# Optimization experiments

Hardware: AMD Instinct MI355X
Metric: run time of the kernel (lower is better)

Reference implementation:

```python
import jax, jax.numpy as jnp
import numpy as np

ALPHA = 0.2      # GAT leaky_relu slope (args.alpha)
MLP_SLOPE = 0.01 # F.leaky_relu default in the MLP path
NEG = -9e15

def _l2_normalize(x, axis=1, eps=1e-12):
    n = jnp.sqrt(jnp.sum(x * x, axis=axis, keepdims=True))
    return x / jnp.maximum(n, eps)

def setup_inputs() -> dict:
    key = jax.random.key(0)
    ks = jax.random.split(key, 14)
    N, Din, Dh, H, Dg, M1, M2, E = 8192, 512, 256, 2, 512, 512, 256, 100000
    x = jax.random.normal(ks[0], (N, Din), dtype=jnp.float32)
    adj = jax.random.randint(ks[1], (N, N), 0, 2, dtype=jnp.int32)
    train_sample = jax.random.randint(ks[2], (E, 2), 0, N, dtype=jnp.int32)
    llm_emb = jax.random.normal(ks[3], (N, Dg), dtype=jnp.float32)
    # GAT head params (stacked over heads)
    Wg = jax.random.normal(ks[4], (H, Din, Dh), dtype=jnp.float32) * 0.05
    a1 = jax.random.normal(ks[5], (H, Dh), dtype=jnp.float32) * 0.05
    a2 = jax.random.normal(ks[6], (H, Dh), dtype=jnp.float32) * 0.05
    bias_g = jnp.zeros((H, Dh), dtype=jnp.float32)
    # MLP params
    W1 = jax.random.normal(ks[7], (Dh + Dg, M1), dtype=jnp.float32) * 0.03
    b1 = jnp.zeros((M1,), dtype=jnp.float32)
    W2 = jax.random.normal(ks[8], (M1, M2), dtype=jnp.float32) * 0.04
    b2 = jnp.zeros((M2,), dtype=jnp.float32)
    return {"x": x, "adj": adj, "train_sample": train_sample, "llm_emb": llm_emb,
            "Wg": Wg, "a1": a1, "a2": a2, "bias_g": bias_g,
            "W1": W1, "b1": b1, "W2": W2, "b2": b2}

def reference(x, adj, train_sample, llm_emb, Wg, a1, a2, bias_g, W1, b1, W2, b2):
    mask = adj > 0  # [N, N]

    def head(W, av1, av2, b):
        h = x @ W                                   # [N, Dh]
        s1 = h @ av1                                # [N]
        s2 = h @ av2                                # [N]
        e = jax.nn.leaky_relu(s1[:, None] + s2[None, :], ALPHA)  # [N, N]
        att = jax.nn.softmax(jnp.where(mask, e, NEG), axis=1)
        out = att @ h                               # [N, Dh]
        out = jax.nn.leaky_relu(out, ALPHA)
        out = _l2_normalize(out, axis=1)
        return out + b

    # encode: single GNN layer -> mean over heads (dropout inactive in eval)
    out_heads = jax.vmap(head)(Wg, a1, a2, bias_g)  # [H, N, Dh]
    embed_gnn = jnp.mean(out_heads, axis=0)         # [N, Dh]
    embed = jnp.concatenate([llm_emb, embed_gnn], axis=1)  # [N, Dg+Dh]

    def mlp(z):
        z = jax.nn.leaky_relu(z @ W1 + b1, MLP_SLOPE)
        z = jax.nn.leaky_relu(z @ W2 + b2, MLP_SLOPE)
        return z

    tf_embed = mlp(embed)
    target_embed = mlp(embed)
    train_tf = tf_embed[train_sample[:, 0]]
    train_tg = target_embed[train_sample[:, 1]]
    pred = jnp.sum(train_tf * train_tg, axis=1, keepdims=True)  # dot decode, [E,1]
    return pred
```

## Files before the change

### kernel.cpp

```cpp
#include <hip/hip_runtime.h>
#include <hip/hip_bf16.h>
#include <cstdint>
#include <cstddef>

#define ALPHA 0.2f
#define MLP_SLOPE 0.01f

typedef short bf16x8 __attribute__((ext_vector_type(8)));
typedef float f32x4 __attribute__((ext_vector_type(4)));
typedef unsigned short ushort_t;

#define ASM_BARRIER() __asm__ __volatile__("s_waitcnt lgkmcnt(0)\n\ts_barrier" ::: "memory")

__device__ __forceinline__ float lrelu(float x, float s) { return x > 0.f ? x : x * s; }
__device__ __forceinline__ ushort_t f2bf(float x) {
  __hip_bfloat16 h = __float2bfloat16(x);
  return *reinterpret_cast<ushort_t*>(&h);
}
__device__ __forceinline__ float bf2f(ushort_t u) {
  union { unsigned int i; float f; } v; v.i = ((unsigned int)u) << 16; return v.f;
}

__global__ __launch_bounds__(256) void tobf(
    const float* __restrict__ in, ushort_t* __restrict__ outp)
{
  int idx = blockIdx.x * 256 + threadIdx.x;
  float4 v = ((const float4*)in)[idx];
  ushort4 h;
  h.x = f2bf(v.x); h.y = f2bf(v.y); h.z = f2bf(v.z); h.w = f2bf(v.w);
  ((ushort4*)outp)[idx] = h;
}

__global__ __launch_bounds__(256) void zero_f(float* __restrict__ p)
{
  int idx = blockIdx.x * 256 + threadIdx.x;
  ((float4*)p)[idx] = make_float4(0.f, 0.f, 0.f, 0.f);
}

__global__ __launch_bounds__(256) void pack_wt(
    const float* __restrict__ W, ushort_t* __restrict__ hi,
    ushort_t* __restrict__ lo, int K, int N)
{
  int gid = blockIdx.x * 256 + threadIdx.x;
  int lane = gid & 63;
  int kbc = K >> 5;
  int kblk = (gid >> 6) % kbc;
  int nblk = (gid >> 6) / kbc;
  size_t b = (size_t)blockIdx.y * K * N;
  int col = nblk * 16 + (lane & 15);
  int krow = kblk * 32 + (lane >> 4) * 8;
  ushort_t h[8] __attribute__((aligned(16)));
  ushort_t l[8] __attribute__((aligned(16)));
#pragma unroll
  for (int e = 0; e < 8; ++e) {
    float v = W[b + (size_t)(krow + e) * N + col];
    h[e] = f2bf(v);
    l[e] = f2bf(v - bf2f(h[e]));
  }
  *(uint4*)&hi[b + (size_t)gid * 8] = *(uint4*)h;
  if (lo) *(uint4*)&lo[b + (size_t)gid * 8] = *(uint4*)l;
}

__global__ __launch_bounds__(256, 2) void gemm_h(
    const ushort_t* __restrict__ xb, const ushort_t* __restrict__ Wgp,
    const float* __restrict__ a1, const float* __restrict__ a2,
    ushort_t* __restrict__ Bpack, float* __restrict__ s1,
    float* __restrict__ s2)
{
  __shared__ ushort_t Ab[2][128][40];
  const int t = threadIdx.x;
  const int head = blockIdx.z;
  const int m0 = blockIdx.y * 128;
  const int n0 = blockIdx.x * 64;
  const int wave = t >> 6;
  const int wm = (wave & 1) * 64, wn = (wave >> 1) * 32;
  const int l16 = t & 15, quad = (t >> 4) & 3, l63 = t & 63;
  const int sr = t >> 1, sp = (t & 1) * 16;
  const ushort_t* arow_g = xb + (size_t)(m0 + sr) * 512 + sp;
  const ushort_t* bp = Wgp + (size_t)head * 256 * 512;
  const int nb0 = (n0 + wn) >> 4;

  f32x4 acc[4][2];
#pragma unroll
  for (int i = 0; i < 4; ++i)
#pragma unroll
    for (int j = 0; j < 2; ++j) acc[i][j] = (f32x4){0.f, 0.f, 0.f, 0.f};

  uint4 r0, r1;
  r0 = *(const uint4*)(arow_g);
  r1 = *(const uint4*)(arow_g + 8);
  *(uint4*)&Ab[0][sr][sp] = r0;
  *(uint4*)&Ab[0][sr][sp + 8] = r1;
  __syncthreads();

  for (int kb = 0; kb < 16; ++kb) {
    const int cur = kb & 1, nxt = cur ^ 1;
    if (kb < 15) {
      const ushort_t* p = arow_g + (kb + 1) * 32;
      r0 = *(const uint4*)p;
      r1 = *(const uint4*)(p + 8);
    }
    bf16x8 Bf[2];
#pragma unroll
    for (int nt = 0; nt < 2; ++nt)
      Bf[nt] = *(const bf16x8*)&bp[(((size_t)(nb0 + nt) * 16 + kb) * 64 + l63) * 8];
    bf16x8 Af[4];
#pragma unroll
    for (int mt = 0; mt < 4; ++mt)
      Af[mt] = *(const bf16x8*)&Ab[cur][wm + mt * 16 + l16][quad * 8];
#pragma unroll
    for (int mt = 0; mt < 4; ++mt)
#pragma unroll
      for (int nt = 0; nt < 2; ++nt)
        acc[mt][nt] = __builtin_amdgcn_mfma_f32_16x16x32_bf16(
            Af[mt], Bf[nt], acc[mt][nt], 0, 0, 0);
    if (kb < 15) {
      *(uint4*)&Ab[nxt][sr][sp] = r0;
      *(uint4*)&Ab[nxt][sr][sp + 8] = r1;
    }
    __syncthreads();
  }

#pragma unroll
  for (int mt = 0; mt < 4; ++mt)
#pragma unroll
    for (int nt = 0; nt < 2; ++nt)
#pragma unroll
      for (int rg = 0; rg < 4; ++rg) {
        int j = m0 + wm + mt * 16 + quad * 4 + rg;
        int c = n0 + wn + nt * 16 + l16;
        int kblk = j >> 5;
        int laneb = ((j >> 3) & 3) * 16 + (c & 15);
        int e = j & 7;
        Bpack[(((size_t)head * 256 + kblk) * 16 + (c >> 4)) * 512 + laneb * 8 + e] =
            f2bf(acc[mt][nt][rg]);
      }
  float a1v[2], a2v[2];
#pragma unroll
  for (int nt = 0; nt < 2; ++nt) {
    int c = n0 + wn + nt * 16 + l16;
    a1v[nt] = a1[head * 256 + c];
    a2v[nt] = a2[head * 256 + c];
  }
#pragma unroll
  for (int mt = 0; mt < 4; ++mt)
#pragma unroll
    for (int rg = 0; rg < 4; ++rg) {
      float p1 = acc[mt][0][rg] * a1v[0] + acc[mt][1][rg] * a1v[1];
      float p2 = acc[mt][0][rg] * a2v[0] + acc[mt][1][rg] * a2v[1];
      p1 += __shfl_xor(p1, 1); p2 += __shfl_xor(p2, 1);
      p1 += __shfl_xor(p1, 2); p2 += __shfl_xor(p2, 2);
      p1 += __shfl_xor(p1, 4); p2 += __shfl_xor(p2, 4);
      p1 += __shfl_xor(p1, 8); p2 += __shfl_xor(p2, 8);
      if (l16 == 0) {
        int row = m0 + wm + mt * 16 + quad * 4 + rg;
        atomicAdd(&s1[head * 8192 + row], p1);
        atomicAdd(&s2[head * 8192 + row], p2);
      }
    }
}

__global__ __launch_bounds__(256, 2) void gemm_mlp(
    const ushort_t* __restrict__ Ahi, const ushort_t* __restrict__ Alo,
    const ushort_t* __restrict__ Bph, const ushort_t* __restrict__ Bpl,
    const float* __restrict__ bias, float* __restrict__ Cf,
    ushort_t* __restrict__ Chi, ushort_t* __restrict__ Clo,
    int M, int N, int K, float slope)
{
  __shared__ ushort_t Ah[2][128][40], Al[2][128][40];
  const int kbc = K >> 5;
  const int t = threadIdx.x;
  const int m0 = blockIdx.y * 128;
  const int n0 = blockIdx.x * 64;
  const int wave = t >> 6;
  const int wm = (wave & 1) * 64, wn = (wave >> 1) * 32;
  const int l16 = t & 15, quad = (t >> 4) & 3, l63 = t & 63;
  const int sr = t >> 1, sp = (t & 1) * 16;
  const ushort_t* ah_g = Ahi + (size_t)(m0 + sr) * K + sp;
  const ushort_t* al_g = Alo + (size_t)(m0 + sr) * K + sp;
  const int nb0 = (n0 + wn) >> 4;

  f32x4 acc[4][2];
#pragma unroll
  for (int i = 0; i < 4; ++i)
#pragma unroll
    for (int j = 0; j < 2; ++j) acc[i][j] = (f32x4){0.f, 0.f, 0.f, 0.f};

  uint4 rh0, rh1, rl0, rl1;
  rh0 = *(const uint4*)(ah_g);
  rh1 = *(const uint4*)(ah_g + 8);
  rl0 = *(const uint4*)(al_g);
  rl1 = *(const uint4*)(al_g + 8);
  *(uint4*)&Ah[0][sr][sp] = rh0;
  *(uint4*)&Ah[0][sr][sp + 8] = rh1;
  *(uint4*)&Al[0][sr][sp] = rl0;
  *(uint4*)&Al[0][sr][sp + 8] = rl1;
  __syncthreads();

  for (int kb = 0; kb < kbc; ++kb) {
    const int cur = kb & 1, nxt = cur ^ 1;
    if (kb + 1 < kbc) {
      const ushort_t* ph = ah_g + (kb + 1) * 32;
      const ushort_t* plo = al_g + (kb + 1) * 32;
      rh0 = *(const uint4*)ph;
      rh1 = *(const uint4*)(ph + 8);
      rl0 = *(const uint4*)plo;
      rl1 = *(const uint4*)(plo + 8);
    }
    bf16x8 bh[2], bl[2];
#pragma unroll
    for (int nt = 0; nt < 2; ++nt) {
      size_t o = (((size_t)(nb0 + nt) * kbc + kb) * 64 + l63) * 8;
      bh[nt] = *(const bf16x8*)&Bph[o];
      bl[nt] = *(const bf16x8*)&Bpl[o];
    }
    bf16x8 afh[4], afl[4];
#pragma unroll
    for (int mt = 0; mt < 4; ++mt) {
      afh[mt] = *(const bf16x8*)&Ah[cur][wm + mt * 16 + l16][quad * 8];
      afl[mt] = *(const bf16x8*)&Al[cur][wm + mt * 16 + l16][quad * 8];
    }
#pragma unroll
    for (int mt = 0; mt < 4; ++mt)
#pragma unroll
      for (int nt = 0; nt < 2; ++nt) {
        acc[mt][nt] = __builtin_amdgcn_mfma_f32_16x16x32_bf16(afh[mt], bh[nt], acc[mt][nt], 0, 0, 0);
        acc[mt][nt] = __builtin_amdgcn_mfma_f32_16x16x32_bf16(afh[mt], bl[nt], acc[mt][nt], 0, 0, 0);
        acc[mt][nt] = __builtin_amdgcn_mfma_f32_16x16x32_bf16(afl[mt], bh[nt], acc[mt][nt], 0, 0, 0);
      }
    if (kb + 1 < kbc) {
      *(uint4*)&Ah[nxt][sr][sp] = rh0;
      *(uint4*)&Ah[nxt][sr][sp + 8] = rh1;
      *(uint4*)&Al[nxt][sr][sp] = rl0;
      *(uint4*)&Al[nxt][sr][sp + 8] = rl1;
    }
    __syncthreads();
  }

#pragma unroll
  for (int mt = 0; mt < 4; ++mt)
#pragma unroll
    for (int nt = 0; nt < 2; ++nt)
#pragma unroll
      for (int rg = 0; rg < 4; ++rg) {
        int m = m0 + wm + mt * 16 + quad * 4 + rg;
        int n = n0 + wn + nt * 16 + l16;
        float v = lrelu(acc[mt][nt][rg] + bias[n], slope);
        size_t o = (size_t)m * N + n;
        if (Cf) Cf[o] = v;
        if (Chi) {
          ushort_t h = f2bf(v);
          Chi[o] = h; Clo[o] = f2bf(v - bf2f(h));
        }
      }
}

__global__ __launch_bounds__(512, 1) void attn_mfma8(
    const ushort_t* __restrict__ Bpack, const float* __restrict__ s1g,
    const float* __restrict__ s2g, const int* __restrict__ adj,
    ushort_t* __restrict__ pacc, float* __restrict__ pl)
{
  __shared__ ushort_t Wlds[2][2][8][64][8];
  const int t = threadIdx.x;
  const int i0 = blockIdx.x * 128;
  const int js = blockIdx.y;
  const int kbase = js * 2048;
  const int wr = t >> 2, kq = t & 3;
  const int glane = kq * 16 + (wr & 15);
  const int gmt = wr >> 4;
  const float s1v0 = s1g[i0 + wr];
  const float s1v1 = s1g[8192 + i0 + wr];
  const int wave = t >> 6;
  const int head = wave >> 2, nh = (wave >> 1) & 1, rg2 = wave & 1;
  const int l16 = t & 15, quad = (t >> 4) & 3;
  const int l63 = t & 63;
  f32x4 acc[4][8];
#pragma unroll
  for (int m = 0; m < 4; ++m)
#pragma unroll
    for (int n = 0; n < 8; ++n) acc[m][n] = (f32x4){0.f, 0.f, 0.f, 0.f};
  float rs0 = 0.f, rs1 = 0.f;

  const int* arow = adj + (size_t)(i0 + wr) * 8192;
  int4 pa0, pa1;
  float4 p20a, p20b, p21a, p21b;

  auto fetch = [&](int kk) {
    pa0 = *(const int4*)&arow[kk];
    pa1 = *(const int4*)&arow[kk + 4];
    p20a = *(const float4*)&s2g[kk];
    p20b = *(const float4*)&s2g[kk + 4];
    p21a = *(const float4*)&s2g[8192 + kk];
    p21b = *(const float4*)&s2g[8192 + kk + 4];
  };
  auto gen = [&](int buf) {
    int am[8] = {pa0.x, pa0.y, pa0.z, pa0.w, pa1.x, pa1.y, pa1.z, pa1.w};
    float s20[8] = {p20a.x, p20a.y, p20a.z, p20a.w, p20b.x, p20b.y, p20b.z, p20b.w};
    float s21[8] = {p21a.x, p21a.y, p21a.z, p21a.w, p21b.x, p21b.y, p21b.z, p21b.w};
    ushort_t w0[8] __attribute__((aligned(16)));
    ushort_t w1[8] __attribute__((aligned(16)));
#pragma unroll
    for (int e = 0; e < 8; ++e) {
      float e0 = s1v0 + s20[e];
      float e1 = s1v1 + s21[e];
      e0 = fmaxf(e0, 0.f) + ALPHA * fminf(e0, 0.f);
      e1 = fmaxf(e1, 0.f) + ALPHA * fminf(e1, 0.f);
      float v0 = am[e] > 0 ? __expf(e0) : 0.f;
      float v1 = am[e] > 0 ? __expf(e1) : 0.f;
      rs0 += v0; rs1 += v1;
      w0[e] = f2bf(v0); w1[e] = f2bf(v1);
    }
    *(uint4*)&Wlds[buf][0][gmt][glane][0] = *(uint4*)w0;
    *(uint4*)&Wlds[buf][1][gmt][glane][0] = *(uint4*)w1;
  };

  fetch(kbase + kq * 8);
  gen(0);
  fetch(kbase + 32 + kq * 8);
  ASM_BARRIER();

  for (int kt = 0; kt < 64; ++kt) {
    const int cur = kt & 1, nxt = cur ^ 1;
    const int kblk = js * 64 + kt;
    const ushort_t* bb =
        Bpack + ((((size_t)head * 256 + kblk) * 16 + nh * 8) * 64 + l63) * 8;
    bf16x8 Bf[8];
#pragma unroll
    for (int nt = 0; nt < 8; ++nt)
      Bf[nt] = *(const bf16x8*)&bb[nt * 512];
    bf16x8 Af[4];
#pragma unroll
    for (int mt = 0; mt < 4; ++mt)
      Af[mt] = *(const bf16x8*)&Wlds[cur][head][rg2 * 4 + mt][l63][0];
#pragma unroll
    for (int mt = 0; mt < 4; ++mt)
#pragma unroll
      for (int nt = 0; nt < 8; ++nt)
        acc[mt][nt] = __builtin_amdgcn_mfma_f32_16x16x32_bf16(
            Af[mt], Bf[nt], acc[mt][nt], 0, 0, 0);
    if (kt < 63) {
      gen(nxt);
      if (kt < 62) fetch(kbase + (kt + 2) * 32 + kq * 8);
    }
    ASM_BARRIER();
  }

  rs0 += __shfl_xor(rs0, 1); rs0 += __shfl_xor(rs0, 2);
  rs1 += __shfl_xor(rs1, 1); rs1 += __shfl_xor(rs1, 2);
  if (kq == 0) {
    pl[((size_t)js * 2 + 0) * 8192 + i0 + wr] = rs0;
    pl[((size_t)js * 2 + 1) * 8192 + i0 + wr] = rs1;
  }
  const int n0 = nh * 128;
#pragma unroll
  for (int mt = 0; mt < 4; ++mt)
#pragma unroll
    for (int nt = 0; nt < 8; ++nt)
#pragma unroll
      for (int rg = 0; rg < 4; ++rg) {
        int row = i0 + rg2 * 64 + mt * 16 + quad * 4 + rg;
        int col = n0 + nt * 16 + l16;
        pacc[(((size_t)js * 2 + head) * 8192 + row) * 256 + col] =
            f2bf(acc[mt][nt][rg]);
      }
}

__global__ __launch_bounds__(256) void attn_finalize(
    const ushort_t* __restrict__ pacc, const float* __restrict__ pl,
    const float* __restrict__ bg, const float* __restrict__ llm,
    ushort_t* __restrict__ ehi, ushort_t* __restrict__ elo)
{
  __shared__ float red[8];
  const int r = blockIdx.x;
  const int t = threadIdx.x;
  const int wv = t >> 6, lane = t & 63;
#pragma unroll
  for (int half = 0; half < 2; ++half) {
    float lv = llm[(size_t)r * 512 + half * 256 + t];
    ushort_t h = f2bf(lv);
    ehi[(size_t)r * 768 + half * 256 + t] = h;
    elo[(size_t)r * 768 + half * 256 + t] = f2bf(lv - bf2f(h));
  }
  float o[2];
#pragma unroll
  for (int hh = 0; hh < 2; ++hh) {
    float num = 0.f, l = 0.f;
#pragma unroll
    for (int js = 0; js < 4; ++js) {
      num += bf2f(pacc[(((size_t)js * 2 + hh) * 8192 + r) * 256 + t]);
      l += pl[((size_t)js * 2 + hh) * 8192 + r];
    }
    o[hh] = lrelu(num / l, ALPHA);
  }
  float v0 = o[0] * o[0], v1 = o[1] * o[1];
  for (int off = 32; off > 0; off >>= 1) {
    v0 += __shfl_xor(v0, off);
    v1 += __shfl_xor(v1, off);
  }
  if (lane == 0) { red[wv] = v0; red[4 + wv] = v1; }
  __syncthreads();
  float n0 = fmaxf(sqrtf(red[0] + red[1] + red[2] + red[3]), 1e-12f);
  float n1 = fmaxf(sqrtf(red[4] + red[5] + red[6] + red[7]), 1e-12f);
  float val = 0.5f * (o[0] / n0 + bg[t] + o[1] / n1 + bg[256 + t]);
  ushort_t h = f2bf(val);
  ehi[(size_t)r * 768 + 512 + t] = h;
  elo[(size_t)r * 768 + 512 + t] = f2bf(val - bf2f(h));
}

__global__ __launch_bounds__(256) void pred_kernel(
    const float* __restrict__ z2, const int* __restrict__ ts,
    float* __restrict__ out, int E)
{
  const int gw = (blockIdx.x * 256 + threadIdx.x) >> 6;
  const int lane = threadIdx.x & 63;
  if (gw >= E) return;
  const int a = ts[gw * 2], b = ts[gw * 2 + 1];
  float4 va = ((const float4*)(z2 + (size_t)a * 256))[lane];
  float4 vb = ((const float4*)(z2 + (size_t)b * 256))[lane];
  float p = va.x * vb.x + va.y * vb.y + va.z * vb.z + va.w * vb.w;
  for (int off = 32; off > 0; off >>= 1) p += __shfl_xor(p, off);
  if (lane == 0) out[gw] = p;
}

extern "C" void kernel_launch(void* const* d_in, const int* in_sizes, int n_in,
                              void* d_out, int out_size, void* d_ws, size_t ws_size,
                              hipStream_t stream) {
  const float* x   = (const float*)d_in[0];
  const int*   adj = (const int*)d_in[1];
  const int*   ts  = (const int*)d_in[2];
  const float* llm = (const float*)d_in[3];
  const float* Wg  = (const float*)d_in[4];
  const float* a1  = (const float*)d_in[5];
  const float* a2  = (const float*)d_in[6];
  const float* bg  = (const float*)d_in[7];
  const float* W1  = (const float*)d_in[8];
  const float* b1  = (const float*)d_in[9];
  const float* W2  = (const float*)d_in[10];
  const float* b2  = (const float*)d_in[11];
  float* out = (float*)d_out;
  float* ws  = (float*)d_ws;
  const int E = in_sizes[2] / 2;

  ushort_t* xb    = (ushort_t*)(ws + 0);
  ushort_t* Wgp   = (ushort_t*)(ws + 2097152);
  ushort_t* W1ph  = (ushort_t*)(ws + 2228224);
  ushort_t* W1pl  = (ushort_t*)(ws + 2424832);
  ushort_t* W2ph  = (ushort_t*)(ws + 2621440);
  ushort_t* W2pl  = (ushort_t*)(ws + 2686976);
  ushort_t* Bpack = (ushort_t*)(ws + 2752512);
  float*    s1    = ws + 4849664;
  float*    s2    = ws + 4866048;
  float*    pl    = ws + 4882432;
  ushort_t* pacc  = (ushort_t*)(ws + 4947968);
  ushort_t* ehi   = (ushort_t*)(ws + 13336576);
  ushort_t* elo   = (ushort_t*)(ws + 16482304);
  ushort_t* z1hi  = (ushort_t*)(ws + 19628032);
  ushort_t* z1lo  = (ushort_t*)(ws + 21725184);
  float*    z2    = ws + 23822336;

  tobf<<<4096, 256, 0, stream>>>(x, xb);
  pack_wt<<<dim3(64, 2), 256, 0, stream>>>(Wg, Wgp, nullptr, 512, 256);
  pack_wt<<<dim3(192, 1), 256, 0, stream>>>(W1, W1ph, W1pl, 768, 512);
  pack_wt<<<dim3(64, 1), 256, 0, stream>>>(W2, W2ph, W2pl, 512, 256);
  zero_f<<<32, 256, 0, stream>>>(s1);
  gemm_h<<<dim3(4, 64, 2), 256, 0, stream>>>(xb, Wgp, a1, a2, Bpack, s1, s2);
  attn_mfma8<<<dim3(64, 4), 512, 0, stream>>>(Bpack, s1, s2, adj, pacc, pl);
  attn_finalize<<<8192, 256, 0, stream>>>(pacc, pl, bg, llm, ehi, elo);
  gemm_mlp<<<dim3(8, 64), 256, 0, stream>>>(
      ehi, elo, W1ph, W1pl, b1, nullptr, z1hi, z1lo, 8192, 512, 768, MLP_SLOPE);
  gemm_mlp<<<dim3(4, 64), 256, 0, stream>>>(
      z1hi, z1lo, W2ph, W2pl, b2, z2, nullptr, nullptr, 8192, 256, 512, MLP_SLOPE);
  pred_kernel<<<(E * 64 + 255) / 256, 256, 0, stream>>>(z2, ts, out, E);
}
```

Measured before the change: 584.5 us.

## Process two k-steps per barrier in attention MFMA loop

Restructures the attention main loop so each iteration handles two 32-wide k-steps, with the LDS weight buffer doubled and two prefetch register sets, halving the number of block-wide barriers. Weight generation for one step is interleaved with the MFMA work of the other, aiming to hide barrier and global-load latency. This costs more LDS and more registers in a kernel already launched with a single block per SM, which could add spills or pressure.

```diff
diff --git a/kernel.cpp b/kernel.cpp
--- a/kernel.cpp
+++ b/kernel.cpp
@@ -260,7 +260,7 @@
     const float* __restrict__ s2g, const int* __restrict__ adj,
     ushort_t* __restrict__ pacc, float* __restrict__ pl)
 {
-  __shared__ ushort_t Wlds[2][2][8][64][8];
+  __shared__ ushort_t Wlds[2][2][2][8][64][8];
   const int t = threadIdx.x;
   const int i0 = blockIdx.x * 128;
   const int js = blockIdx.y;
@@ -282,21 +282,25 @@
   float rs0 = 0.f, rs1 = 0.f;
 
   const int* arow = adj + (size_t)(i0 + wr) * 8192;
-  int4 pa0, pa1;
-  float4 p20a, p20b, p21a, p21b;
-
-  auto fetch = [&](int kk) {
-    pa0 = *(const int4*)&arow[kk];
-    pa1 = *(const int4*)&arow[kk + 4];
-    p20a = *(const float4*)&s2g[kk];
-    p20b = *(const float4*)&s2g[kk + 4];
-    p21a = *(const float4*)&s2g[8192 + kk];
-    p21b = *(const float4*)&s2g[8192 + kk + 4];
+
+  struct FS { int4 pa0, pa1; float4 p20a, p20b, p21a, p21b; };
+  FS fsA, fsB;
+
+  auto fetch = [&](FS& f, int kk) {
+    f.pa0 = *(const int4*)&arow[kk];
+    f.pa1 = *(const int4*)&arow[kk + 4];
+    f.p20a = *(const float4*)&s2g[kk];
+    f.p20b = *(const float4*)&s2g[kk + 4];
+    f.p21a = *(const float4*)&s2g[8192 + kk];
+    f.p21b = *(const float4*)&s2g[8192 + kk + 4];
   };
-  auto gen = [&](int buf) {
-    int am[8] = {pa0.x, pa0.y, pa0.z, pa0.w, pa1.x, pa1.y, pa1.z, pa1.w};
-    float s20[8] = {p20a.x, p20a.y, p20a.z, p20a.w, p20b.x, p20b.y, p20b.z, p20b.w};
-    float s21[8] = {p21a.x, p21a.y, p21a.z, p21a.w, p21b.x, p21b.y, p21b.z, p21b.w};
+  auto gen = [&](const FS& f, int buf, int step) {
+    int am[8] = {f.pa0.x, f.pa0.y, f.pa0.z, f.pa0.w,
+                 f.pa1.x, f.pa1.y, f.pa1.z, f.pa1.w};
+    float s20[8] = {f.p20a.x, f.p20a.y, f.p20a.z, f.p20a.w,
+                    f.p20b.x, f.p20b.y, f.p20b.z, f.p20b.w};
+    float s21[8] = {f.p21a.x, f.p21a.y, f.p21a.z, f.p21a.w,
+                    f.p21b.x, f.p21b.y, f.p21b.z, f.p21b.w};
     ushort_t w0[8] __attribute__((aligned(16)));
     ushort_t w1[8] __attribute__((aligned(16)));
 #pragma unroll
@@ -310,17 +314,10 @@
       rs0 += v0; rs1 += v1;
       w0[e] = f2bf(v0); w1[e] = f2bf(v1);
     }
-    *(uint4*)&Wlds[buf][0][gmt][glane][0] = *(uint4*)w0;
-    *(uint4*)&Wlds[buf][1][gmt][glane][0] = *(uint4*)w1;
+    *(uint4*)&Wlds[buf][step][0][gmt][glane][0] = *(uint4*)w0;
+    *(uint4*)&Wlds[buf][step][1][gmt][glane][0] = *(uint4*)w1;
   };
-
-  fetch(kbase + kq * 8);
-  gen(0);
-  fetch(kbase + 32 + kq * 8);
-  ASM_BARRIER();
-
-  for (int kt = 0; kt < 64; ++kt) {
-    const int cur = kt & 1, nxt = cur ^ 1;
+  auto mstep = [&](int buf, int step, int kt) {
     const int kblk = js * 64 + kt;
     const ushort_t* bb =
         Bpack + ((((size_t)head * 256 + kblk) * 16 + nh * 8) * 64 + l63) * 8;
@@ -331,16 +328,32 @@
     bf16x8 Af[4];
 #pragma unroll
     for (int mt = 0; mt < 4; ++mt)
-      Af[mt] = *(const bf16x8*)&Wlds[cur][head][rg2 * 4 + mt][l63][0];
+      Af[mt] = *(const bf16x8*)&Wlds[buf][step][head][rg2 * 4 + mt][l63][0];
 #pragma unroll
     for (int mt = 0; mt < 4; ++mt)
 #pragma unroll
       for (int nt = 0; nt < 8; ++nt)
         acc[mt][nt] = __builtin_amdgcn_mfma_f32_16x16x32_bf16(
             Af[mt], Bf[nt], acc[mt][nt], 0, 0, 0);
-    if (kt < 63) {
-      gen(nxt);
-      if (kt < 62) fetch(kbase + (kt + 2) * 32 + kq * 8);
+  };
+
+  fetch(fsA, kbase + kq * 8);
+  fetch(fsB, kbase + 32 + kq * 8);
+  gen(fsA, 0, 0);
+  gen(fsB, 0, 1);
+  fetch(fsA, kbase + 64 + kq * 8);
+  fetch(fsB, kbase + 96 + kq * 8);
+  ASM_BARRIER();
+
+  for (int p = 0; p < 32; ++p) {
+    const int cur = p & 1, nxt = cur ^ 1;
+    mstep(cur, 0, 2 * p);
+    if (p < 31) gen(fsA, nxt, 0);
+    mstep(cur, 1, 2 * p + 1);
+    if (p < 31) gen(fsB, nxt, 1);
+    if (p < 30) {
+      fetch(fsA, kbase + (2 * p + 4) * 32 + kq * 8);
+      fetch(fsB, kbase + (2 * p + 5) * 32 + kq * 8);
     }
     ASM_BARRIER();
   }
```

New measurement: 593.3 us. About the same (+1.5%).

## Halve attention row tile, split weight generation by head, raise occupancy

Applied to the files above, without the earlier changes.

The attention kernel now handles 64 rows per block instead of 128, and the grid doubles to 128x4 blocks. Each half of the 512 threads generates exp-weights for one head rather than every thread computing both heads. The accumulator shrinks from 4x8 to 2x8 tiles, and launch bounds ask for 4 blocks per CU to raise occupancy and latency hiding. B fragments are software-prefetched one at a time instead of all eight loaded up front, which cuts register pressure. The trade-off is that each Bpack fragment is reused by fewer rows, so global/L2 traffic for B roughly doubles.

```diff
diff --git a/kernel.cpp b/kernel.cpp
--- a/kernel.cpp
+++ b/kernel.cpp
@@ -255,63 +255,73 @@
       }
 }
 
-__global__ __launch_bounds__(512, 1) void attn_mfma8(
+__global__ __launch_bounds__(512, 4) void attn_mfma8(
     const ushort_t* __restrict__ Bpack, const float* __restrict__ s1g,
     const float* __restrict__ s2g, const int* __restrict__ adj,
     ushort_t* __restrict__ pacc, float* __restrict__ pl)
 {
-  __shared__ ushort_t Wlds[2][2][8][64][8];
+  __shared__ ushort_t Wlds[2][2][4][64][8];
   const int t = threadIdx.x;
-  const int i0 = blockIdx.x * 128;
+  const int i0 = blockIdx.x * 64;
   const int js = blockIdx.y;
   const int kbase = js * 2048;
-  const int wr = t >> 2, kq = t & 3;
+  const int ghead = t >> 8;
+  const int wr = (t & 255) >> 2, kq = t & 3;
   const int glane = kq * 16 + (wr & 15);
   const int gmt = wr >> 4;
-  const float s1v0 = s1g[i0 + wr];
-  const float s1v1 = s1g[8192 + i0 + wr];
+  const float s1v = s1g[ghead * 8192 + i0 + wr];
+  const float* s2h = s2g + ghead * 8192;
   const int wave = t >> 6;
-  const int head = wave >> 2, nh = (wave >> 1) & 1, rg2 = wave & 1;
+  const int chead = wave >> 2, nh = (wave >> 1) & 1, rg2 = wave & 1;
   const int l16 = t & 15, quad = (t >> 4) & 3;
   const int l63 = t & 63;
-  f32x4 acc[4][8];
-#pragma unroll
-  for (int m = 0; m < 4; ++m)
+  f32x4 acc[2][8];
+#pragma unroll
+  for (int m = 0; m < 2; ++m)
 #pragma unroll
     for (int n = 0; n < 8; ++n) acc[m][n] = (f32x4){0.f, 0.f, 0.f, 0.f};
-  float rs0 = 0.f, rs1 = 0.f;
+  float rs = 0.f;
 
   const int* arow = adj + (size_t)(i0 + wr) * 8192;
   int4 pa0, pa1;
-  float4 p20a, p20b, p21a, p21b;
+  float4 p2a, p2b;
 
   auto fetch = [&](int kk) {
     pa0 = *(const int4*)&arow[kk];
     pa1 = *(const int4*)&arow[kk + 4];
-    p20a = *(const float4*)&s2g[kk];
-    p20b = *(const float4*)&s2g[kk + 4];
-    p21a = *(const float4*)&s2g[8192 + kk];
-    p21b = *(const float4*)&s2g[8192 + kk + 4];
+    p2a = *(const float4*)&s2h[kk];
+    p2b = *(const float4*)&s2h[kk + 4];
   };
   auto gen = [&](int buf) {
     int am[8] = {pa0.x, pa0.y, pa0.z, pa0.w, pa1.x, pa1.y, pa1.z, pa1.w};
-    float s20[8] = {p20a.x, p20a.y, p20a.z, p20a.w, p20b.x, p20b.y, p20b.z, p20b.w};
-    float s21[8] = {p21a.x, p21a.y, p21a.z, p21a.w, p21b.x, p21b.y, p21b.z, p21b.w};
+    float s2v[8] = {p2a.x, p2a.y, p2a.z, p2a.w, p2b.x, p2b.y, p2b.z, p2b.w};
     ushort_t w0[8] __attribute__((aligned(16)));
-    ushort_t w1[8] __attribute__((aligned(16)));
 #pragma unroll
     for (int e = 0; e < 8; ++e) {
-      float e0 = s1v0 + s20[e];
-      float e1 = s1v1 + s21[e];
+      float e0 = s1v + s2v[e];
       e0 = fmaxf(e0, 0.f) + ALPHA * fminf(e0, 0.f);
-      e1 = fmaxf(e1, 0.f) + ALPHA * fminf(e1, 0.f);
       float v0 = am[e] > 0 ? __expf(e0) : 0.f;
-      float v1 = am[e] > 0 ? __expf(e1) : 0.f;
-      rs0 += v0; rs1 += v1;
-      w0[e] = f2bf(v0); w1[e] = f2bf(v1);
-    }
-    *(uint4*)&Wlds[buf][0][gmt][glane][0] = *(uint4*)w0;
-    *(uint4*)&Wlds[buf][1][gmt][glane][0] = *(uint4*)w1;
+      rs += v0;
+      w0[e] = f2bf(v0);
+    }
+    *(uint4*)&Wlds[buf][ghead][gmt][glane][0] = *(uint4*)w0;
+  };
+  auto mstep = [&](int buf, int kt) {
+    const int kblk = js * 64 + kt;
+    const ushort_t* bb =
+        Bpack + ((((size_t)chead * 256 + kblk) * 16 + nh * 8) * 64 + l63) * 8;
+    bf16x8 Af0 = *(const bf16x8*)&Wlds[buf][chead][rg2 * 2 + 0][l63][0];
+    bf16x8 Af1 = *(const bf16x8*)&Wlds[buf][chead][rg2 * 2 + 1][l63][0];
+    bf16x8 b0 = *(const bf16x8*)&bb[0];
+#pragma unroll
+    for (int nt = 0; nt < 8; ++nt) {
+      bf16x8 bcur = b0;
+      if (nt < 7) b0 = *(const bf16x8*)&bb[(nt + 1) * 512];
+      acc[0][nt] = __builtin_amdgcn_mfma_f32_16x16x32_bf16(
+          Af0, bcur, acc[0][nt], 0, 0, 0);
+      acc[1][nt] = __builtin_amdgcn_mfma_f32_16x16x32_bf16(
+          Af1, bcur, acc[1][nt], 0, 0, 0);
+    }
   };
 
   fetch(kbase + kq * 8);
@@ -321,23 +331,7 @@
 
   for (int kt = 0; kt < 64; ++kt) {
     const int cur = kt & 1, nxt = cur ^ 1;
-    const int kblk = js * 64 + kt;
-    const ushort_t* bb =
-        Bpack + ((((size_t)head * 256 + kblk) * 16 + nh * 8) * 64 + l63) * 8;
-    bf16x8 Bf[8];
-#pragma unroll
-    for (int nt = 0; nt < 8; ++nt)
-      Bf[nt] = *(const bf16x8*)&bb[nt * 512];
-    bf16x8 Af[4];
-#pragma unroll
-    for (int mt = 0; mt < 4; ++mt)
-      Af[mt] = *(const bf16x8*)&Wlds[cur][head][rg2 * 4 + mt][l63][0];
-#pragma unroll
-    for (int mt = 0; mt < 4; ++mt)
-#pragma unroll
-      for (int nt = 0; nt < 8; ++nt)
-        acc[mt][nt] = __builtin_amdgcn_mfma_f32_16x16x32_bf16(
-            Af[mt], Bf[nt], acc[mt][nt], 0, 0, 0);
+    mstep(cur, kt);
     if (kt < 63) {
       gen(nxt);
       if (kt < 62) fetch(kbase + (kt + 2) * 32 + kq * 8);
@@ -345,22 +339,19 @@
     ASM_BARRIER();
   }
 
-  rs0 += __shfl_xor(rs0, 1); rs0 += __shfl_xor(rs0, 2);
-  rs1 += __shfl_xor(rs1, 1); rs1 += __shfl_xor(rs1, 2);
-  if (kq == 0) {
-    pl[((size_t)js * 2 + 0) * 8192 + i0 + wr] = rs0;
-    pl[((size_t)js * 2 + 1) * 8192 + i0 + wr] = rs1;
-  }
+  rs += __shfl_xor(rs, 1); rs += __shfl_xor(rs, 2);
+  if (kq == 0)
+    pl[((size_t)js * 2 + ghead) * 8192 + i0 + wr] = rs;
   const int n0 = nh * 128;
 #pragma unroll
-  for (int mt = 0; mt < 4; ++mt)
+  for (int mt = 0; mt < 2; ++mt)
 #pragma unroll
     for (int nt = 0; nt < 8; ++nt)
 #pragma unroll
       for (int rg = 0; rg < 4; ++rg) {
-        int row = i0 + rg2 * 64 + mt * 16 + quad * 4 + rg;
+        int row = i0 + rg2 * 32 + mt * 16 + quad * 4 + rg;
         int col = n0 + nt * 16 + l16;
-        pacc[(((size_t)js * 2 + head) * 8192 + row) * 256 + col] =
+        pacc[(((size_t)js * 2 + chead) * 8192 + row) * 256 + col] =
             f2bf(acc[mt][nt][rg]);
       }
 }
@@ -464,7 +455,7 @@
   pack_wt<<<dim3(64, 1), 256, 0, stream>>>(W2, W2ph, W2pl, 512, 256);
   zero_f<<<32, 256, 0, stream>>>(s1);
   gemm_h<<<dim3(4, 64, 2), 256, 0, stream>>>(xb, Wgp, a1, a2, Bpack, s1, s2);
-  attn_mfma8<<<dim3(64, 4), 512, 0, stream>>>(Bpack, s1, s2, adj, pacc, pl);
+  attn_mfma8<<<dim3(128, 4), 512, 0, stream>>>(Bpack, s1, s2, adj, pacc, pl);
   attn_finalize<<<8192, 256, 0, stream>>>(pacc, pl, bg, llm, ehi, elo);
   gemm_mlp<<<dim3(8, 64), 256, 0, stream>>>(
       ehi, elo, W1ph, W1pl, b1, nullptr, z1hi, z1lo, 8192, 512, 768, MLP_SLOPE);
```

Measured after the change: 623.9 us. +6.7%, slower.
